# Kernel tuning notes

Hardware: AMD Instinct MI355X
Metric: run time of the kernel (lower is better)

## Reference

```python
import jax, jax.numpy as jnp
import numpy as np

N = 16384
E = 524288
F_IN, F_HID, F_OUT = 128, 256, 128
EPS = 1e-5


def setup_inputs() -> dict:
    key = jax.random.key(0)
    ks = jax.random.split(key, 8)
    x = jax.random.normal(ks[0], (N, F_IN), dtype=jnp.float32)
    edge_index = jax.random.randint(ks[1], (2, E), 0, N, dtype=jnp.int64)
    edge_weight = jax.random.uniform(ks[2], (E,), dtype=jnp.float32)
    # Linear params stored as [in, out] (y = x @ W + b; same math as torch Linear)
    W1_w = jax.random.normal(ks[3], (F_IN, F_HID), dtype=jnp.float32) / np.sqrt(F_IN)
    W1_b = jnp.zeros((F_HID,), dtype=jnp.float32)
    W2_w = jax.random.normal(ks[4], (F_HID, F_OUT), dtype=jnp.float32) / np.sqrt(F_HID)
    W2_b = jnp.zeros((F_OUT,), dtype=jnp.float32)
    ln_g = jnp.ones((F_HID,), dtype=jnp.float32)
    ln_b = jnp.zeros((F_HID,), dtype=jnp.float32)
    return {"x": x, "edge_index": edge_index, "edge_weight": edge_weight,
            "W1_w": W1_w, "W1_b": W1_b, "W2_w": W2_w, "W2_b": W2_b,
            "ln_g": ln_g, "ln_b": ln_b}


def _layernorm(h, g, b):
    mu = jnp.mean(h, axis=-1, keepdims=True)
    var = jnp.var(h, axis=-1, keepdims=True)
    return (h - mu) * jax.lax.rsqrt(var + EPS) * g + b


def reference(x, edge_index, edge_weight, W1_w, W1_b, W2_w, W2_b, ln_g, ln_b):
    n = x.shape[0]
    adj = jnp.zeros((n, n), dtype=x.dtype).at[edge_index[0], edge_index[1]].set(edge_weight)
    adj = adj + jnp.eye(n, dtype=x.dtype)
    degree = jnp.clip(adj.sum(axis=1, keepdims=True), 1.0, None)
    adj = adj / degree
    h = jnp.matmul(adj, x) @ W1_w + W1_b          # [N, F_HID]
    h = jax.nn.relu(_layernorm(h, ln_g, ln_b))
    # dropout is identity in eval mode
    out = jnp.matmul(adj, h) @ W2_w + W2_b        # [N, F_OUT]
    return out
```

## Files before the change

### kernel.cpp

```cpp
#include <hip/hip_runtime.h>

#define N_NODES 16384
#define F_IN    128
#define F_HID   256
#define F_OUT   128
#define LN_EPS  1e-5f
#define CAP     128
#define H0STR   136
#define H1STR   264
#define REPSTR  132
#define PLANEU  (N_NODES * 32)

typedef __attribute__((ext_vector_type(8))) short bf16x8;
typedef __attribute__((ext_vector_type(4))) float f32x4;
typedef __attribute__((ext_vector_type(4))) int   i32x4;

__device__ __forceinline__ unsigned short bf16rne(float f) {
    unsigned u = __float_as_uint(f);
    unsigned r = (u + 0x7fffu + ((u >> 16) & 1u)) >> 16;
    return (unsigned short)r;
}
__device__ __forceinline__ float bf_lo(unsigned v) { return __uint_as_float(v << 16); }
__device__ __forceinline__ float bf_hi(unsigned v) { return __uint_as_float(v & 0xffff0000u); }

__global__ void pre_small_kernel(int* __restrict__ cur, const unsigned* __restrict__ ei,
                                 int* __restrict__ mode) {
    int b = blockIdx.x, t = threadIdx.x;
    if (b < 64) {
        cur[b * 256 + t] = 0;
    } else {
        __shared__ int nz;
        if (t == 0) nz = 0;
        __syncthreads();
        for (int it = 0; it < 4; ++it) {
            int idx = 2 * (t + it * 256) + 1;
            if (ei[idx] != 0u) nz = 1;
        }
        __syncthreads();
        if (t == 0) *mode = (nz == 0) ? 1 : 0;
    }
}

__global__ void prep_fill_kernel(const void* __restrict__ ei, const int* __restrict__ mode,
                                 int* __restrict__ cur, int2* __restrict__ ed, int E, int nF,
                                 const float* __restrict__ x, unsigned short* __restrict__ xb,
                                 const float* __restrict__ W1, unsigned short* __restrict__ W1t,
                                 const float* __restrict__ W2, unsigned short* __restrict__ W2t) {
    int b = blockIdx.x, t = threadIdx.x;
    if (b < nF) {
        int base = b * 1024 + t;
        int m = *mode;
#pragma unroll
        for (int u = 0; u < 4; ++u) {
            int e = base + u * 256;
            if (e >= E) continue;
            int r, c;
            if (m) {
                const long long* p = (const long long*)ei;
                r = (int)p[e]; c = (int)p[e + E];
            } else {
                const int* p = (const int*)ei;
                r = p[e]; c = p[e + E];
            }
            if (((unsigned)r | (unsigned)c) >= N_NODES) continue;
            int pos = atomicAdd(&cur[r], 1);
            if (pos < CAP) ed[r * CAP + pos] = make_int2(c, e);
        }
    } else if (b < nF + 2048) {
        int i = ((b - nF) * 256 + t) * 4;
        float4 v = *(const float4*)&x[i];
        ushort4 o;
        o.x = bf16rne(v.x); o.y = bf16rne(v.y); o.z = bf16rne(v.z); o.w = bf16rne(v.w);
        int n = i >> 7, f = i & 127;
        int p = f >> 6, fo = f & 63;
        *(ushort4*)&xb[(size_t)p * (N_NODES * 64) + n * 64 + fo] = o;
    } else if (b < nF + 2176) {
        int id = (b - nF - 2048) * 256 + t;
        int n = id >> 7, k = id & 127;
        W1t[id] = bf16rne(W1[(size_t)k * F_HID + n]);
    } else {
        int id = (b - nF - 2176) * 256 + t;
        int n = id >> 8, k = id & 255;
        W2t[id] = bf16rne(W2[(size_t)k * F_OUT + n]);
    }
}

__launch_bounds__(1024, 8)
__global__ void agg_mlp_kernel(const float* __restrict__ ew, int* __restrict__ cur,
                               int2* __restrict__ ed, float* __restrict__ invdeg,
                               const unsigned* __restrict__ xb,
                               const unsigned short* __restrict__ W1t,
                               const unsigned short* __restrict__ W2t,
                               const float* __restrict__ b1,
                               const float* __restrict__ ln_g, const float* __restrict__ ln_b,
                               unsigned short* __restrict__ h2b) {
    __shared__ int   scol[16][CAP];
    __shared__ int   seid[16][CAP];
    __shared__ float sw[16][CAP];
    __shared__ unsigned short H0[16 * H0STR];
    __shared__ unsigned short H1[16 * H1STR];
    __shared__ float red[2][16][16];

    int t = threadIdx.x, wave = t >> 6, lane = t & 63;
    int lnid = lane & 15, quad = lane >> 4;
    int half = lane >> 5, hl = lane & 31;
    int Rbase = blockIdx.x * 16;
    int r = Rbase + wave;

    int d = cur[r];
    if (d > CAP) d = CAP;
    int dpad = (d + 15) & ~15;
    int2* row = ed + (size_t)r * CAP;
    for (int i = lane; i < d; i += 64) {
        int2 e = row[i];
        scol[wave][i] = e.x;
        seid[wave][i] = e.y;
    }
    for (int i = d + lane; i < dpad; i += 64) {
        scol[wave][i] = -2;
        seid[wave][i] = 0;
    }
    asm volatile("s_waitcnt lgkmcnt(0)" ::: "memory");

    float wsum = 0.0f;
    for (int i = lane; i < d; i += 64) {
        int myc = scol[wave][i], mye = seid[wave][i];
        bool kill = false;
        for (int jb = 0; jb < dpad; jb += 16) {
            const int* cb = &scol[wave][jb];
            const int* eb = &seid[wave][jb];
            i32x4 c0 = *(const i32x4*)(cb);
            i32x4 c1 = *(const i32x4*)(cb + 4);
            i32x4 c2 = *(const i32x4*)(cb + 8);
            i32x4 c3 = *(const i32x4*)(cb + 12);
            i32x4 e0 = *(const i32x4*)(eb);
            i32x4 e1 = *(const i32x4*)(eb + 4);
            i32x4 e2 = *(const i32x4*)(eb + 8);
            i32x4 e3 = *(const i32x4*)(eb + 12);
            kill |= (c0.x == myc && e0.x > mye);
            kill |= (c0.y == myc && e0.y > mye);
            kill |= (c0.z == myc && e0.z > mye);
            kill |= (c0.w == myc && e0.w > mye);
            kill |= (c1.x == myc && e1.x > mye);
            kill |= (c1.y == myc && e1.y > mye);
            kill |= (c1.z == myc && e1.z > mye);
            kill |= (c1.w == myc && e1.w > mye);
            kill |= (c2.x == myc && e2.x > mye);
            kill |= (c2.y == myc && e2.y > mye);
            kill |= (c2.z == myc && e2.z > mye);
            kill |= (c2.w == myc && e2.w > mye);
            kill |= (c3.x == myc && e3.x > mye);
            kill |= (c3.y == myc && e3.y > mye);
            kill |= (c3.z == myc && e3.z > mye);
            kill |= (c3.w == myc && e3.w > mye);
        }
        float w = kill ? 0.0f : ew[mye];
        sw[wave][i] = w;
        row[i] = make_int2(myc, __float_as_int(w));
        wsum += w;
    }
    asm volatile("s_waitcnt lgkmcnt(0)" ::: "memory");
    for (int off = 32; off; off >>= 1) wsum += __shfl_xor(wsum, off, 64);
    float inv = 1.0f / (1.0f + wsum);
    if (lane == 0) { invdeg[r] = inv; cur[r] = d; }

    float selfw = half ? 0.0f : 1.0f;
#pragma unroll 1
    for (int p = 0; p < 2; ++p) {
        const unsigned* xp = xb + (size_t)p * PLANEU;
        unsigned sv = xp[r * 32 + hl];
        float a0 = selfw * bf_lo(sv), a1 = selfw * bf_hi(sv);
        int j = 0;
        for (; j + 16 <= d; j += 16) {
            int c[8]; float w[8]; unsigned v[8];
#pragma unroll
            for (int u = 0; u < 8; ++u) {
                c[u] = scol[wave][j + 2 * u + half];
                w[u] = sw[wave][j + 2 * u + half];
            }
#pragma unroll
            for (int u = 0; u < 8; ++u) v[u] = xp[c[u] * 32 + hl];
#pragma unroll
            for (int u = 0; u < 8; ++u) {
                a0 += w[u] * bf_lo(v[u]); a1 += w[u] * bf_hi(v[u]);
            }
        }
        for (; j + 2 <= d; j += 2) {
            int cc = scol[wave][j + half];
            float w = sw[wave][j + half];
            unsigned v = xp[cc * 32 + hl];
            a0 += w * bf_lo(v); a1 += w * bf_hi(v);
        }
        if (j < d) {
            int cc = scol[wave][j];
            float w = half ? 0.0f : sw[wave][j];
            unsigned v = xp[cc * 32 + hl];
            a0 += w * bf_lo(v); a1 += w * bf_hi(v);
        }
        a0 += __shfl_xor(a0, 32, 64);
        a1 += __shfl_xor(a1, 32, 64);
        if (half == 0) {
            unsigned w0 = ((unsigned)bf16rne(a1 * inv) << 16) | (unsigned)bf16rne(a0 * inv);
            *(unsigned*)&H0[wave * H0STR + p * 64 + hl * 2] = w0;
        }
        __syncthreads();
    }

    bf16x8 a[4];
#pragma unroll
    for (int ch = 0; ch < 4; ++ch)
        a[ch] = *(const bf16x8*)&H0[lnid * H0STR + ch * 32 + quad * 8];
    f32x4 acc = {0.0f, 0.0f, 0.0f, 0.0f};
    {
        const unsigned short* wrow = &W1t[(size_t)(wave * 16 + lnid) * F_IN];
#pragma unroll
        for (int ch = 0; ch < 4; ++ch) {
            bf16x8 b = *(const bf16x8*)&wrow[ch * 32 + quad * 8];
            acc = __builtin_amdgcn_mfma_f32_16x16x32_bf16(a[ch], b, acc, 0, 0, 0);
        }
    }
    float s[4], q[4];
    {
        float bv = b1[wave * 16 + lnid];
#pragma unroll
        for (int rr = 0; rr < 4; ++rr) {
            float v = acc[rr] + bv;
            acc[rr] = v;
            s[rr] = v; q[rr] = v * v;
        }
    }
#pragma unroll
    for (int rr = 0; rr < 4; ++rr)
        for (int off = 1; off < 16; off <<= 1) {
            s[rr] += __shfl_xor(s[rr], off, 64);
            q[rr] += __shfl_xor(q[rr], off, 64);
        }
    if (lnid == 0) {
#pragma unroll
        for (int rr = 0; rr < 4; ++rr) {
            red[0][wave][quad * 4 + rr] = s[rr];
            red[1][wave][quad * 4 + rr] = q[rr];
        }
    }
    __syncthreads();
    float mean[4], rinv[4];
#pragma unroll
    for (int rr = 0; rr < 4; ++rr) {
        int rowi = quad * 4 + rr;
        float S = 0.0f, Q = 0.0f;
#pragma unroll
        for (int w2 = 0; w2 < 16; ++w2) { S += red[0][w2][rowi]; Q += red[1][w2][rowi]; }
        mean[rr] = S * (1.0f / F_HID);
        float var = Q * (1.0f / F_HID) - mean[rr] * mean[rr];
        rinv[rr] = rsqrtf(var + LN_EPS);
    }
    {
        int c = wave * 16 + lnid;
        float g = ln_g[c], bb = ln_b[c];
#pragma unroll
        for (int rr = 0; rr < 4; ++rr) {
            float v = fmaxf((acc[rr] - mean[rr]) * rinv[rr] * g + bb, 0.0f);
            H1[(quad * 4 + rr) * H1STR + c] = bf16rne(v);
        }
    }
    __syncthreads();

    unsigned short* rep = H0;
    if (wave < 8) {
        bf16x8 a2[8];
#pragma unroll
        for (int ch = 0; ch < 8; ++ch)
            a2[ch] = *(const bf16x8*)&H1[lnid * H1STR + ch * 32 + quad * 8];
        f32x4 c2 = {0.0f, 0.0f, 0.0f, 0.0f};
        const unsigned short* wrow = &W2t[(size_t)(wave * 16 + lnid) * F_HID];
#pragma unroll
        for (int ch = 0; ch < 8; ++ch) {
            bf16x8 b = *(const bf16x8*)&wrow[ch * 32 + quad * 8];
            c2 = __builtin_amdgcn_mfma_f32_16x16x32_bf16(a2[ch], b, c2, 0, 0, 0);
        }
#pragma unroll
        for (int rr = 0; rr < 4; ++rr)
            rep[(quad * 4 + rr) * REPSTR + wave * 16 + lnid] = bf16rne(c2[rr]);
    }
    __syncthreads();

    if (t < 512) {
        int m = t >> 5, cg = t & 31;
        int p = cg >> 4, fo = (cg & 15) * 4;
        *(ushort4*)&h2b[(size_t)p * (N_NODES * 64) + (size_t)(Rbase + m) * 64 + fo] =
            *(const ushort4*)&rep[m * REPSTR + cg * 4];
    }
}

__launch_bounds__(1024, 8)
__global__ void spmm2_kernel(const unsigned* __restrict__ xb, const int* __restrict__ cur,
                             const int2* __restrict__ ed, const float* __restrict__ invdeg,
                             const float* __restrict__ bias, float* __restrict__ outp) {
    __shared__ int   scol[16][CAP];
    __shared__ float sw[16][CAP];
    int t = threadIdx.x, wave = t >> 6, lane = t & 63;
    int half = lane >> 5, hl = lane & 31;
    int r = blockIdx.x * 16 + wave;
    const int2* row = ed + (size_t)r * CAP;
    int d = cur[r];
    if (d > CAP) d = CAP;
    for (int i = lane; i < d; i += 64) {
        int2 e = row[i];
        scol[wave][i] = e.x;
        sw[wave][i] = __int_as_float(e.y);
    }
    asm volatile("s_waitcnt lgkmcnt(0)" ::: "memory");

    float inv = invdeg[r];
    float selfw = half ? 0.0f : 1.0f;
#pragma unroll 1
    for (int p = 0; p < 2; ++p) {
        const unsigned* xp = xb + (size_t)p * PLANEU;
        unsigned sv = xp[r * 32 + hl];
        float a0 = selfw * bf_lo(sv), a1 = selfw * bf_hi(sv);
        int j = 0;
        for (; j + 16 <= d; j += 16) {
            int c[8]; float w[8]; unsigned v[8];
#pragma unroll
            for (int u = 0; u < 8; ++u) {
                c[u] = scol[wave][j + 2 * u + half];
                w[u] = sw[wave][j + 2 * u + half];
            }
#pragma unroll
            for (int u = 0; u < 8; ++u) v[u] = xp[c[u] * 32 + hl];
#pragma unroll
            for (int u = 0; u < 8; ++u) {
                a0 += w[u] * bf_lo(v[u]); a1 += w[u] * bf_hi(v[u]);
            }
        }
        for (; j + 2 <= d; j += 2) {
            int cc = scol[wave][j + half];
            float w = sw[wave][j + half];
            unsigned v = xp[cc * 32 + hl];
            a0 += w * bf_lo(v); a1 += w * bf_hi(v);
        }
        if (j < d) {
            int cc = scol[wave][j];
            float w = half ? 0.0f : sw[wave][j];
            unsigned v = xp[cc * 32 + hl];
            a0 += w * bf_lo(v); a1 += w * bf_hi(v);
        }
        a0 += __shfl_xor(a0, 32, 64);
        a1 += __shfl_xor(a1, 32, 64);
        if (half == 0) {
            int f = p * 64 + 2 * hl;
            float2 o;
            o.x = a0 * inv + bias[f];
            o.y = a1 * inv + bias[f + 1];
            *(float2*)&outp[(size_t)r * F_OUT + f] = o;
        }
        __syncthreads();
    }
}

extern "C" void kernel_launch(void* const* d_in, const int* in_sizes, int n_in,
                              void* d_out, int out_size, void* d_ws, size_t ws_size,
                              hipStream_t stream) {
    const float* x   = (const float*)d_in[0];
    const void*  ei  = d_in[1];
    const float* ew  = (const float*)d_in[2];
    const float* W1  = (const float*)d_in[3];
    const float* b1  = (const float*)d_in[4];
    const float* W2  = (const float*)d_in[5];
    const float* b2  = (const float*)d_in[6];
    const float* lng = (const float*)d_in[7];
    const float* lnb = (const float*)d_in[8];
    float* out = (float*)d_out;
    int E = in_sizes[2];

    char* w = (char*)d_ws;
    size_t off = 0;
    auto take = [&](size_t bytes) -> char* {
        char* p = w + off;
        off += (bytes + 255) & ~(size_t)255;
        return p;
    };
    int*   cur    = (int*)take((size_t)N_NODES * 4);
    float* invdeg = (float*)take((size_t)N_NODES * 4);
    int2*  ed     = (int2*)take((size_t)N_NODES * CAP * 8);
    unsigned short* xb  = (unsigned short*)take((size_t)N_NODES * F_IN * 2);
    unsigned short* h2b = (unsigned short*)take((size_t)N_NODES * F_OUT * 2);
    unsigned short* W1t = (unsigned short*)take((size_t)F_IN * F_HID * 2);
    unsigned short* W2t = (unsigned short*)take((size_t)F_HID * F_OUT * 2);
    int*   mode   = (int*)take(4);

    int nF = (E + 1023) / 1024;
    pre_small_kernel<<<65, 256, 0, stream>>>(cur, (const unsigned*)ei, mode);
    prep_fill_kernel<<<nF + 2304, 256, 0, stream>>>(ei, mode, cur, ed, E, nF,
                                                    x, xb, W1, W1t, W2, W2t);
    agg_mlp_kernel<<<N_NODES / 16, 1024, 0, stream>>>(ew, cur, ed, invdeg,
                                                      (const unsigned*)xb, W1t, W2t,
                                                      b1, lng, lnb, h2b);
    spmm2_kernel<<<N_NODES / 16, 1024, 0, stream>>>((const unsigned*)h2b, cur, ed, invdeg,
                                                    b2, out);
}
```

Measured before the change: 195.0 us.

## Use row-major bf16 feature layout with 16-byte gathers in SpMM kernels

Drops the two-plane split feature layout for x and h2 and stores them row-major, 256 bytes per node. Each aggregation pass now gathers a whole neighbor row with 16-byte loads, handling four neighbors per wave instead of two, in one pass with no per-plane loop or barrier. This cuts the number of gather instructions and the repeated reads of index and weight data. In exchange it needs more accumulator registers and a two-step cross-lane reduction, and tail handling now covers remainders of up to three neighbors.

```diff
diff --git a/kernel.cpp b/kernel.cpp
--- a/kernel.cpp
+++ b/kernel.cpp
@@ -9,11 +9,11 @@
 #define H0STR   136
 #define H1STR   264
 #define REPSTR  132
-#define PLANEU  (N_NODES * 32)
 
 typedef __attribute__((ext_vector_type(8))) short bf16x8;
 typedef __attribute__((ext_vector_type(4))) float f32x4;
 typedef __attribute__((ext_vector_type(4))) int   i32x4;
+typedef __attribute__((ext_vector_type(4))) unsigned u32x4;
 
 __device__ __forceinline__ unsigned short bf16rne(float f) {
     unsigned u = __float_as_uint(f);
@@ -71,9 +71,7 @@
         float4 v = *(const float4*)&x[i];
         ushort4 o;
         o.x = bf16rne(v.x); o.y = bf16rne(v.y); o.z = bf16rne(v.z); o.w = bf16rne(v.w);
-        int n = i >> 7, f = i & 127;
-        int p = f >> 6, fo = f & 63;
-        *(ushort4*)&xb[(size_t)p * (N_NODES * 64) + n * 64 + fo] = o;
+        *(ushort4*)&xb[i] = o;
     } else if (b < nF + 2176) {
         int id = (b - nF - 2048) * 256 + t;
         int n = id >> 7, k = id & 127;
@@ -103,7 +101,7 @@
 
     int t = threadIdx.x, wave = t >> 6, lane = t & 63;
     int lnid = lane & 15, quad = lane >> 4;
-    int half = lane >> 5, hl = lane & 31;
+    int qw = lane >> 4, ql = lane & 15;
     int Rbase = blockIdx.x * 16;
     int r = Rbase + wave;
 
@@ -164,59 +162,79 @@
     float inv = 1.0f / (1.0f + wsum);
     if (lane == 0) { invdeg[r] = inv; cur[r] = d; }
 
-    float selfw = half ? 0.0f : 1.0f;
-#pragma unroll 1
-    for (int p = 0; p < 2; ++p) {
-        const unsigned* xp = xb + (size_t)p * PLANEU;
-        unsigned sv = xp[r * 32 + hl];
-        float a0 = selfw * bf_lo(sv), a1 = selfw * bf_hi(sv);
-        int j = 0;
-        for (; j + 16 <= d; j += 16) {
-            int c[8]; float w[8]; unsigned v[8];
-#pragma unroll
-            for (int u = 0; u < 8; ++u) {
-                c[u] = scol[wave][j + 2 * u + half];
-                w[u] = sw[wave][j + 2 * u + half];
+    const u32x4* xb4 = (const u32x4*)xb;
+    float a[8] = {0, 0, 0, 0, 0, 0, 0, 0};
+    int j = 0;
+    for (; j + 16 <= d; j += 16) {
+        int c[4]; float w[4]; u32x4 v[4];
+#pragma unroll
+        for (int u = 0; u < 4; ++u) {
+            int n = j + u * 4 + qw;
+            c[u] = scol[wave][n];
+            w[u] = sw[wave][n];
+        }
+#pragma unroll
+        for (int u = 0; u < 4; ++u) v[u] = xb4[(size_t)c[u] * 16 + ql];
+#pragma unroll
+        for (int u = 0; u < 4; ++u)
+#pragma unroll
+            for (int m = 0; m < 4; ++m) {
+                a[2 * m]     += w[u] * bf_lo(v[u][m]);
+                a[2 * m + 1] += w[u] * bf_hi(v[u][m]);
             }
-#pragma unroll
-            for (int u = 0; u < 8; ++u) v[u] = xp[c[u] * 32 + hl];
-#pragma unroll
-            for (int u = 0; u < 8; ++u) {
-                a0 += w[u] * bf_lo(v[u]); a1 += w[u] * bf_hi(v[u]);
-            }
-        }
-        for (; j + 2 <= d; j += 2) {
-            int cc = scol[wave][j + half];
-            float w = sw[wave][j + half];
-            unsigned v = xp[cc * 32 + hl];
-            a0 += w * bf_lo(v); a1 += w * bf_hi(v);
-        }
-        if (j < d) {
-            int cc = scol[wave][j];
-            float w = half ? 0.0f : sw[wave][j];
-            unsigned v = xp[cc * 32 + hl];
-            a0 += w * bf_lo(v); a1 += w * bf_hi(v);
-        }
-        a0 += __shfl_xor(a0, 32, 64);
-        a1 += __shfl_xor(a1, 32, 64);
-        if (half == 0) {
-            unsigned w0 = ((unsigned)bf16rne(a1 * inv) << 16) | (unsigned)bf16rne(a0 * inv);
-            *(unsigned*)&H0[wave * H0STR + p * 64 + hl * 2] = w0;
-        }
-        __syncthreads();
-    }
-
-    bf16x8 a[4];
+    }
+    for (; j + 4 <= d; j += 4) {
+        int n = j + qw;
+        int c = scol[wave][n];
+        float w = sw[wave][n];
+        u32x4 v = xb4[(size_t)c * 16 + ql];
+#pragma unroll
+        for (int m = 0; m < 4; ++m) {
+            a[2 * m]     += w * bf_lo(v[m]);
+            a[2 * m + 1] += w * bf_hi(v[m]);
+        }
+    }
+    int rem = d - j;
+    if (rem > 0) {
+        int n = j + (qw < rem ? qw : 0);
+        float w = (qw < rem) ? sw[wave][n] : 0.0f;
+        int c = scol[wave][n];
+        u32x4 v = xb4[(size_t)c * 16 + ql];
+#pragma unroll
+        for (int m = 0; m < 4; ++m) {
+            a[2 * m]     += w * bf_lo(v[m]);
+            a[2 * m + 1] += w * bf_hi(v[m]);
+        }
+    }
+#pragma unroll
+    for (int k = 0; k < 8; ++k) {
+        a[k] += __shfl_xor(a[k], 16, 64);
+        a[k] += __shfl_xor(a[k], 32, 64);
+    }
+    if (qw == 0) {
+        u32x4 sv = xb4[(size_t)r * 16 + ql];
+        u32x4 o;
+#pragma unroll
+        for (int m = 0; m < 4; ++m) {
+            float lo = (a[2 * m]     + bf_lo(sv[m])) * inv;
+            float hi = (a[2 * m + 1] + bf_hi(sv[m])) * inv;
+            o[m] = ((unsigned)bf16rne(hi) << 16) | (unsigned)bf16rne(lo);
+        }
+        *(u32x4*)&H0[wave * H0STR + ql * 8] = o;
+    }
+    __syncthreads();
+
+    bf16x8 afr[4];
 #pragma unroll
     for (int ch = 0; ch < 4; ++ch)
-        a[ch] = *(const bf16x8*)&H0[lnid * H0STR + ch * 32 + quad * 8];
+        afr[ch] = *(const bf16x8*)&H0[lnid * H0STR + ch * 32 + quad * 8];
     f32x4 acc = {0.0f, 0.0f, 0.0f, 0.0f};
     {
         const unsigned short* wrow = &W1t[(size_t)(wave * 16 + lnid) * F_IN];
 #pragma unroll
         for (int ch = 0; ch < 4; ++ch) {
             bf16x8 b = *(const bf16x8*)&wrow[ch * 32 + quad * 8];
-            acc = __builtin_amdgcn_mfma_f32_16x16x32_bf16(a[ch], b, acc, 0, 0, 0);
+            acc = __builtin_amdgcn_mfma_f32_16x16x32_bf16(afr[ch], b, acc, 0, 0, 0);
         }
     }
     float s[4], q[4];
@@ -286,8 +304,7 @@
 
     if (t < 512) {
         int m = t >> 5, cg = t & 31;
-        int p = cg >> 4, fo = (cg & 15) * 4;
-        *(ushort4*)&h2b[(size_t)p * (N_NODES * 64) + (size_t)(Rbase + m) * 64 + fo] =
+        *(ushort4*)&h2b[(size_t)(Rbase + m) * F_OUT + cg * 4] =
             *(const ushort4*)&rep[m * REPSTR + cg * 4];
     }
 }
@@ -299,7 +316,7 @@
     __shared__ int   scol[16][CAP];
     __shared__ float sw[16][CAP];
     int t = threadIdx.x, wave = t >> 6, lane = t & 63;
-    int half = lane >> 5, hl = lane & 31;
+    int qw = lane >> 4, ql = lane & 15;
     int r = blockIdx.x * 16 + wave;
     const int2* row = ed + (size_t)r * CAP;
     int d = cur[r];
@@ -311,50 +328,72 @@
     }
     asm volatile("s_waitcnt lgkmcnt(0)" ::: "memory");
 
-    float inv = invdeg[r];
-    float selfw = half ? 0.0f : 1.0f;
-#pragma unroll 1
-    for (int p = 0; p < 2; ++p) {
-        const unsigned* xp = xb + (size_t)p * PLANEU;
-        unsigned sv = xp[r * 32 + hl];
-        float a0 = selfw * bf_lo(sv), a1 = selfw * bf_hi(sv);
-        int j = 0;
-        for (; j + 16 <= d; j += 16) {
-            int c[8]; float w[8]; unsigned v[8];
-#pragma unroll
-            for (int u = 0; u < 8; ++u) {
-                c[u] = scol[wave][j + 2 * u + half];
-                w[u] = sw[wave][j + 2 * u + half];
+    const u32x4* xb4 = (const u32x4*)xb;
+    float a[8] = {0, 0, 0, 0, 0, 0, 0, 0};
+    int j = 0;
+    for (; j + 16 <= d; j += 16) {
+        int c[4]; float w[4]; u32x4 v[4];
+#pragma unroll
+        for (int u = 0; u < 4; ++u) {
+            int n = j + u * 4 + qw;
+            c[u] = scol[wave][n];
+            w[u] = sw[wave][n];
+        }
+#pragma unroll
+        for (int u = 0; u < 4; ++u) v[u] = xb4[(size_t)c[u] * 16 + ql];
+#pragma unroll
+        for (int u = 0; u < 4; ++u)
+#pragma unroll
+            for (int m = 0; m < 4; ++m) {
+                a[2 * m]     += w[u] * bf_lo(v[u][m]);
+                a[2 * m + 1] += w[u] * bf_hi(v[u][m]);
             }
-#pragma unroll
-            for (int u = 0; u < 8; ++u) v[u] = xp[c[u] * 32 + hl];
-#pragma unroll
-            for (int u = 0; u < 8; ++u) {
-                a0 += w[u] * bf_lo(v[u]); a1 += w[u] * bf_hi(v[u]);
-            }
-        }
-        for (; j + 2 <= d; j += 2) {
-            int cc = scol[wave][j + half];
-            float w = sw[wave][j + half];
-            unsigned v = xp[cc * 32 + hl];
-            a0 += w * bf_lo(v); a1 += w * bf_hi(v);
-        }
-        if (j < d) {
-            int cc = scol[wave][j];
-            float w = half ? 0.0f : sw[wave][j];
-            unsigned v = xp[cc * 32 + hl];
-            a0 += w * bf_lo(v); a1 += w * bf_hi(v);
-        }
-        a0 += __shfl_xor(a0, 32, 64);
-        a1 += __shfl_xor(a1, 32, 64);
-        if (half == 0) {
-            int f = p * 64 + 2 * hl;
-            float2 o;
-            o.x = a0 * inv + bias[f];
-            o.y = a1 * inv + bias[f + 1];
-            *(float2*)&outp[(size_t)r * F_OUT + f] = o;
-        }
-        __syncthreads();
+    }
+    for (; j + 4 <= d; j += 4) {
+        int n = j + qw;
+        int c = scol[wave][n];
+        float w = sw[wave][n];
+        u32x4 v = xb4[(size_t)c * 16 + ql];
+#pragma unroll
+        for (int m = 0; m < 4; ++m) {
+            a[2 * m]     += w * bf_lo(v[m]);
+            a[2 * m + 1] += w * bf_hi(v[m]);
+        }
+    }
+    int rem = d - j;
+    if (rem > 0) {
+        int n = j + (qw < rem ? qw : 0);
+        float w = (qw < rem) ? sw[wave][n] : 0.0f;
+        int c = scol[wave][n];
+        u32x4 v = xb4[(size_t)c * 16 + ql];
+#pragma unroll
+        for (int m = 0; m < 4; ++m) {
+            a[2 * m]     += w * bf_lo(v[m]);
+            a[2 * m + 1] += w * bf_hi(v[m]);
+        }
+    }
+#pragma unroll
+    for (int k = 0; k < 8; ++k) {
+        a[k] += __shfl_xor(a[k], 16, 64);
+        a[k] += __shfl_xor(a[k], 32, 64);
+    }
+    if (qw == 0) {
+        float inv = invdeg[r];
+        u32x4 sv = xb4[(size_t)r * 16 + ql];
+        int f = ql * 8;
+        f32x4 o0, o1;
+#pragma unroll
+        for (int m = 0; m < 2; ++m) {
+            o0[2 * m]     = (a[2 * m]     + bf_lo(sv[m])) * inv + bias[f + 2 * m];
+            o0[2 * m + 1] = (a[2 * m + 1] + bf_hi(sv[m])) * inv + bias[f + 2 * m + 1];
+        }
+#pragma unroll
+        for (int m = 2; m < 4; ++m) {
+            o1[2 * m - 4] = (a[2 * m]     + bf_lo(sv[m])) * inv + bias[f + 2 * m];
+            o1[2 * m - 3] = (a[2 * m + 1] + bf_hi(sv[m])) * inv + bias[f + 2 * m + 1];
+        }
+        *(f32x4*)&outp[(size_t)r * F_OUT + f]     = o0;
+        *(f32x4*)&outp[(size_t)r * F_OUT + f + 4] = o1;
     }
 }
 
```

Result: faster. 182.2 us, median of 2 (-6.5%).
